# Kernel tuning notes

Hardware: AMD Instinct MI355X
Metric: run time of the kernel (lower is better)

Reference implementation:

```python
import jax, jax.numpy as jnp
import numpy as np

N = 30000      # nodes
D = 512        # nhid
E = 300000     # edges (before self-loops)
P_FEAT = 0.5   # feature dropout (F.dropout, training=True)
P_ATT = 0.6    # GATConv attention dropout
NEG_SLOPE = 0.2
SCALE = 1.0    # PairNorm scale


def setup_inputs() -> dict:
    key = jax.random.key(0)
    k1, k2, k3, k4, k5, k6 = jax.random.split(key, 6)
    x = jax.random.normal(k1, (N, D), dtype=jnp.float32)
    edge_index = jax.random.randint(k2, (2, E), 0, N, dtype=jnp.int32)
    # GATConv params (heads=1): lin weight, att_src/att_dst vectors, bias
    W = jax.random.normal(k3, (D, D), dtype=jnp.float32) * 0.05
    att_src = jax.random.normal(k4, (D,), dtype=jnp.float32) * 0.05
    att_dst = jax.random.normal(k5, (D,), dtype=jnp.float32) * 0.05
    bias = jax.random.normal(k6, (D,), dtype=jnp.float32) * 0.05
    return {"x": x, "edge_index": edge_index, "W": W,
            "att_src": att_src, "att_dst": att_dst, "bias": bias}


def reference(x, edge_index, W, att_src, att_dst, bias):
    # deterministic dropout masks (module runs with training=True)
    dk = jax.random.key(42)
    k_feat, k_att = jax.random.split(dk)

    # F.dropout(x, 0.5, training=True)
    keep = jax.random.bernoulli(k_feat, 1.0 - P_FEAT, x.shape)
    x = jnp.where(keep, x / (1.0 - P_FEAT), jnp.float32(0.0))

    # GATConv(heads=1): linear transform
    h = x @ W                                     # [N, D]

    # add self-loops (PyG default add_self_loops=True)
    src, dst = edge_index[0], edge_index[1]
    loop = jnp.arange(N, dtype=src.dtype)
    src = jnp.concatenate([src, loop])            # [E+N]
    dst = jnp.concatenate([dst, loop])

    # per-edge attention logits: LeakyReLU(a_src . h_j + a_dst . h_i)
    a_s = h @ att_src                             # [N]
    a_d = h @ att_dst                             # [N]
    e = jax.nn.leaky_relu(a_s[src] + a_d[dst], NEG_SLOPE)   # [E+N]

    # segment softmax over incoming edges of each dst node
    m = jax.ops.segment_max(e, dst, num_segments=N)
    m = jnp.where(jnp.isfinite(m), m, jnp.float32(0.0))
    ee = jnp.exp(e - m[dst])
    s = jax.ops.segment_sum(ee, dst, num_segments=N)
    alpha = ee / (s[dst] + 1e-16)                 # [E+N]

    # attention dropout p=0.6
    keep_a = jax.random.bernoulli(k_att, 1.0 - P_ATT, alpha.shape)
    alpha = jnp.where(keep_a, alpha / (1.0 - P_ATT), jnp.float32(0.0))

    # scatter-aggregate weighted messages, add bias
    out = jax.ops.segment_sum(alpha[:, None] * h[src], dst, num_segments=N) + bias

    # PairNorm 'PN': center columns, scale by mean row norm
    out = out - jnp.mean(out, axis=0)
    rownorm_mean = jnp.sqrt(1e-6 + jnp.mean(jnp.sum(out * out, axis=1)))
    out = SCALE * out / rownorm_mean

    return jax.nn.relu(out)
```

## Files before the change

### kernel.cpp

```cpp
#include <hip/hip_runtime.h>
#include <stdint.h>
#include <math.h>


#define N_NODES 30000
#define MPAD    30080
#define DIM     512
#define NEDGE   300000
#define ETOT    330000
#define AGG_BLOCKS 7500
#define RED_BLOCKS 60
#define RED_ROWS   125

#define GEMM_BLOCKS 940
#define CVT_BLOCKS  256
#define DROP_BLOCKS 7520
#define HIST_BLOCKS 1290
#define DOT_BLOCKS  118

#define STILES 118

typedef unsigned int u32;
typedef unsigned short u16;

typedef __attribute__((ext_vector_type(8))) short bf16x8;
typedef __attribute__((ext_vector_type(4))) float f32x4;

__host__ __device__ __forceinline__ void threefry2x32(u32 k0, u32 k1, u32 x0, u32 x1,
                                                      u32& o0, u32& o1) {
  u32 ks2 = k0 ^ k1 ^ 0x1BD11BDAu;
#define TF_R(r) { x0 += x1; x1 = (x1 << r) | (x1 >> (32 - r)); x1 ^= x0; }
  x0 += k0; x1 += k1;
  TF_R(13) TF_R(15) TF_R(26) TF_R(6)
  x0 += k1; x1 += ks2 + 1u;
  TF_R(17) TF_R(29) TF_R(16) TF_R(24)
  x0 += ks2; x1 += k0 + 2u;
  TF_R(13) TF_R(15) TF_R(26) TF_R(6)
  x0 += k0; x1 += k1 + 3u;
  TF_R(17) TF_R(29) TF_R(16) TF_R(24)
  x0 += k1; x1 += ks2 + 4u;
  TF_R(13) TF_R(15) TF_R(26) TF_R(6)
  x0 += ks2; x1 += k0 + 5u;
#undef TF_R
  o0 = x0; o1 = x1;
}

__device__ __forceinline__ u32 tf_fold(u32 k0, u32 k1, u32 idx) {
  u32 a, b;
  threefry2x32(k0, k1, 0u, idx, a, b);
  return a ^ b;
}

__device__ __forceinline__ float bf2f(u32 bits16) {
  return __uint_as_float(bits16 << 16);
}
__device__ __forceinline__ u16 f2bf(float f) {
  u32 u = __float_as_uint(f);
  return (u16)((u + 0x7fffu + ((u >> 16) & 1u)) >> 16);
}

__global__ __launch_bounds__(256) void k_pre(const float* __restrict__ W,
                                             u16* __restrict__ Wt,
                                             const float* __restrict__ x,
                                             u16* __restrict__ xd,
                                             const int* __restrict__ ei,
                                             int* __restrict__ counts,
                                             unsigned int* __restrict__ done,
                                             u32 kf0, u32 kf1) {
  __shared__ u16 tile[32][33];
  int b = blockIdx.x;
  if (b == 0 && threadIdx.x == 0) *done = 0u;
  if (b < CVT_BLOCKS) {
    int bk = (b & 15) * 32, bn = (b >> 4) * 32;
    int c = threadIdx.x & 31, r = threadIdx.x >> 5;
#pragma unroll
    for (int rr = 0; rr < 32; rr += 8)
      tile[r + rr][c] = f2bf(W[(size_t)(bk + r + rr) * DIM + bn + c]);
    __syncthreads();
#pragma unroll
    for (int rr = 0; rr < 32; rr += 8)
      Wt[(size_t)(bn + r + rr) * DIM + bk + c] = tile[c][r + rr];
  } else if (b < CVT_BLOCKS + DROP_BLOCKS) {
    size_t gid = (size_t)(b - CVT_BLOCKS) * 256 + threadIdx.x;
    size_t i0 = gid * 8;
    if (i0 < (size_t)MPAD * DIM) {
      uint4 o = make_uint4(0u, 0u, 0u, 0u);
      if (i0 < (size_t)N_NODES * DIM) {
        float4 v0 = *(const float4*)(x + i0);
        float4 v1 = *(const float4*)(x + i0 + 4);
        float xv[8] = {v0.x, v0.y, v0.z, v0.w, v1.x, v1.y, v1.z, v1.w};
        u32 res[4];
#pragma unroll
        for (int p = 0; p < 4; p++) {
          u32 b0 = tf_fold(kf0, kf1, (u32)i0 + 2 * p);
          u32 b1 = tf_fold(kf0, kf1, (u32)i0 + 2 * p + 1);
          u32 r0 = (b0 >> 31) ? 0u : (u32)f2bf(2.0f * xv[2 * p]);
          u32 r1 = (b1 >> 31) ? 0u : (u32)f2bf(2.0f * xv[2 * p + 1]);
          res[p] = r0 | (r1 << 16);
        }
        o = make_uint4(res[0], res[1], res[2], res[3]);
      }
      *(uint4*)(xd + i0) = o;
    }
  } else {
    int i = (b - CVT_BLOCKS - DROP_BLOCKS) * 256 + threadIdx.x;
    if (i < ETOT) {
      int d = (i < NEDGE) ? ei[NEDGE + i] : (i - NEDGE);
      atomicAdd(&counts[d], 1);
    }
  }
}

__global__ __launch_bounds__(256) void k_gemm(const u16* __restrict__ A,
                                              const u16* __restrict__ B,
                                              u16* __restrict__ H,
                                              const float* __restrict__ atts,
                                              const float* __restrict__ attd,
                                              float* __restrict__ aspart,
                                              float* __restrict__ adpart,
                                              const int* __restrict__ counts,
                                              int* __restrict__ off,
                                              int* __restrict__ cursor) {
  __shared__ __align__(16) u16 lA[128 * 32];
  __shared__ __align__(16) u16 lB[128 * 32];

  if (blockIdx.x == 0) {
    int* tsum = (int*)lA;
    int tid = threadIdx.x, lane = tid & 63, wid = tid >> 6;

    for (int t0 = wid; t0 < STILES; t0 += 32) {
      int4 v[8];
#pragma unroll
      for (int b = 0; b < 8; b++) {
        int t = t0 + b * 4;
        int i = t * 256 + lane * 4;
        if (t < STILES) {
          if (i + 4 <= N_NODES) {
            v[b] = *(const int4*)(counts + i);
          } else {
            v[b].x = (i     < N_NODES) ? counts[i]     : 0;
            v[b].y = (i + 1 < N_NODES) ? counts[i + 1] : 0;
            v[b].z = (i + 2 < N_NODES) ? counts[i + 2] : 0;
            v[b].w = (i + 3 < N_NODES) ? counts[i + 3] : 0;
          }
        } else {
          v[b] = make_int4(0, 0, 0, 0);
        }
      }
#pragma unroll
      for (int b = 0; b < 8; b++) {
        int t = t0 + b * 4;
        if (t < STILES) {
          int s = v[b].x + v[b].y + v[b].z + v[b].w;
#pragma unroll
          for (int d = 1; d < 64; d <<= 1) s += __shfl_xor(s, d);
          if (lane == 0) tsum[t] = s;
        }
      }
    }
    __syncthreads();

    if (wid == 0) {
      int carry = 0;
#pragma unroll
      for (int r = 0; r < 2; r++) {
        int idx = r * 64 + lane;
        int vv = (idx < STILES) ? tsum[idx] : 0;
        int x = vv;
#pragma unroll
        for (int d = 1; d < 64; d <<= 1) {
          int y = __shfl_up(x, d);
          if (lane >= d) x += y;
        }
        if (idx < STILES) tsum[idx] = x - vv + carry;
        carry += __shfl(x, 63);
      }
    }
    __syncthreads();

    for (int t0 = wid; t0 < STILES; t0 += 32) {
      int4 v[8];
#pragma unroll
      for (int b = 0; b < 8; b++) {
        int t = t0 + b * 4;
        int i = t * 256 + lane * 4;
        if (t < STILES) {
          if (i + 4 <= N_NODES) {
            v[b] = *(const int4*)(counts + i);
          } else {
            v[b].x = (i     < N_NODES) ? counts[i]     : 0;
            v[b].y = (i + 1 < N_NODES) ? counts[i + 1] : 0;
            v[b].z = (i + 2 < N_NODES) ? counts[i + 2] : 0;
            v[b].w = (i + 3 < N_NODES) ? counts[i + 3] : 0;
          }
        } else {
          v[b] = make_int4(0, 0, 0, 0);
        }
      }
#pragma unroll
      for (int b = 0; b < 8; b++) {
        int t = t0 + b * 4;
        if (t >= STILES) continue;
        int i = t * 256 + lane * 4;
        int s4 = v[b].x + v[b].y + v[b].z + v[b].w;
        int x = s4;
#pragma unroll
        for (int d = 1; d < 64; d <<= 1) {
          int y = __shfl_up(x, d);
          if (lane >= d) x += y;
        }
        int base = tsum[t] + (x - s4);
        int4 e;
        e.x = base;
        e.y = base + v[b].x;
        e.z = e.y + v[b].y;
        e.w = e.z + v[b].z;
        if (i + 4 <= N_NODES) {
          *(int4*)(off + i) = e;
          *(int4*)(cursor + i) = e;
        } else {
          if (i     < N_NODES) { off[i]     = e.x; cursor[i]     = e.x; }
          if (i + 1 < N_NODES) { off[i + 1] = e.y; cursor[i + 1] = e.y; }
          if (i + 2 < N_NODES) { off[i + 2] = e.z; cursor[i + 2] = e.z; }
          if (i + 3 < N_NODES) { off[i + 3] = e.w; cursor[i + 3] = e.w; }
        }
      }
    }
    if (tid == 0) off[N_NODES] = ETOT;
    return;
  }

  const int g = blockIdx.x - 1;
  const int xcd = g & 7, gi = g >> 3;
  const int wrk = (xcd < 4 ? xcd * 118 : 472 + (xcd - 4) * 117) + gi;

  const int bn = (wrk & 3) * 128;
  const int bm = (wrk >> 2) * 128;
  const int tid = threadIdx.x;
  const int wave = tid >> 6, lane = tid & 63;
  const int quad = lane >> 4, l16 = lane & 15;
  const int wrow = (wave & 1) * 64, wcol = (wave >> 1) * 64;

  f32x4 acc[4][4] = {};
  const int srow = tid >> 2;
  const int scq  = (tid & 3) * 8;

  for (int k0 = 0; k0 < DIM; k0 += 32) {
    uint4 va0 = *(const uint4*)(A + (size_t)(bm + srow) * DIM + k0 + scq);
    uint4 va1 = *(const uint4*)(A + (size_t)(bm + 64 + srow) * DIM + k0 + scq);
    uint4 vb0 = *(const uint4*)(B + (size_t)(bn + srow) * DIM + k0 + scq);
    uint4 vb1 = *(const uint4*)(B + (size_t)(bn + 64 + srow) * DIM + k0 + scq);
    __syncthreads();
    *(uint4*)(lA + srow * 32 + scq) = va0;
    *(uint4*)(lA + (64 + srow) * 32 + scq) = va1;
    *(uint4*)(lB + srow * 32 + scq) = vb0;
    *(uint4*)(lB + (64 + srow) * 32 + scq) = vb1;
    __syncthreads();

    bf16x8 af[4], bfr[4];
#pragma unroll
    for (int i = 0; i < 4; i++)
      af[i] = *(const bf16x8*)(lA + (wrow + i * 16 + l16) * 32 + quad * 8);
#pragma unroll
    for (int j = 0; j < 4; j++)
      bfr[j] = *(const bf16x8*)(lB + (wcol + j * 16 + l16) * 32 + quad * 8);
#pragma unroll
    for (int i = 0; i < 4; i++)
#pragma unroll
      for (int j = 0; j < 4; j++)
        acc[i][j] = __builtin_amdgcn_mfma_f32_16x16x32_bf16(af[i], bfr[j], acc[i][j], 0, 0, 0);
  }

#pragma unroll
  for (int i = 0; i < 4; i++) {
#pragma unroll
    for (int r = 0; r < 4; r++) {
      int row = bm + wrow + i * 16 + quad * 4 + r;
      u16* hp = H + (size_t)row * DIM + bn + wcol + l16;
#pragma unroll
      for (int j = 0; j < 4; j++) hp[j * 16] = f2bf(acc[i][j][r]);
    }
  }

  float as_j[4], ad_j[4];
#pragma unroll
  for (int j = 0; j < 4; j++) {
    int col = bn + wcol + j * 16 + l16;
    as_j[j] = atts[col];
    ad_j[j] = attd[col];
  }
  int slot = ((bn >> 7) << 1) + (wcol >> 6);
#pragma unroll
  for (int i = 0; i < 4; i++) {
#pragma unroll
    for (int r = 0; r < 4; r++) {
      float ps = acc[i][0][r] * as_j[0] + acc[i][1][r] * as_j[1]
               + acc[i][2][r] * as_j[2] + acc[i][3][r] * as_j[3];
      float pd = acc[i][0][r] * ad_j[0] + acc[i][1][r] * ad_j[1]
               + acc[i][2][r] * ad_j[2] + acc[i][3][r] * ad_j[3];
#pragma unroll
      for (int d = 1; d < 16; d <<= 1) {
        ps += __shfl_xor(ps, d);
        pd += __shfl_xor(pd, d);
      }
      int row = bm + wrow + i * 16 + quad * 4 + r;
      if (l16 == 0) {
        aspart[slot * MPAD + row] = ps;
        adpart[slot * MPAD + row] = pd;
      }
    }
  }
}

__global__ __launch_bounds__(256) void k_mid(const float* __restrict__ aspart,
                                             const float* __restrict__ adpart,
                                             float* __restrict__ a_s,
                                             float* __restrict__ a_d,
                                             const int* __restrict__ ei,
                                             int* __restrict__ cursor,
                                             int* __restrict__ perm) {
  int b = blockIdx.x;
  if (b < DOT_BLOCKS) {
    int i = b * 256 + threadIdx.x;
    if (i < N_NODES) {
      float s = 0.f, d = 0.f;
#pragma unroll
      for (int k = 0; k < 8; k++) {
        s += aspart[k * MPAD + i];
        d += adpart[k * MPAD + i];
      }
      a_s[i] = s;
      a_d[i] = d;
    }
  } else {
    int i = (b - DOT_BLOCKS) * 256 + threadIdx.x;
    if (i < ETOT) {
      int d = (i < NEDGE) ? ei[NEDGE + i] : (i - NEDGE);
      int slot = atomicAdd(&cursor[d], 1);
      perm[slot] = i;
    }
  }
}

__global__ __launch_bounds__(256) void k_aggregate(
    const int* __restrict__ ei, const int* __restrict__ off, const int* __restrict__ perm,
    const float* __restrict__ a_s, const float* __restrict__ a_d,
    const u16* __restrict__ h, const float* __restrict__ bias,
    u16* __restrict__ oa, float* __restrict__ colpart,
    float* __restrict__ ssqpart, u32 ka0, u32 ka1) {
  __shared__ float lbuf[4][512];
  int wid = threadIdx.x >> 6;
  int node = blockIdx.x * 4 + wid;
  int lane = threadIdx.x & 63;
  int beg = off[node], end = off[node + 1];
  int deg = end - beg;
  float adn = a_d[node];

  float acc[8] = {0.f, 0.f, 0.f, 0.f, 0.f, 0.f, 0.f, 0.f};

  if (deg <= 64) {
    int idx = beg + lane;
    bool valid = idx < end;
    int s = 0;
    float lg = -3.0e38f;
    u32 keepbits = 0;
    if (valid) {
      int eid = perm[idx];
      s = (eid < NEDGE) ? ei[eid] : (eid - NEDGE);
      lg = a_s[s] + adn;
      lg = (lg < 0.f) ? 0.2f * lg : lg;
      keepbits = tf_fold(ka0, ka1, (u32)eid);
    }
    float mx = lg;
#pragma unroll
    for (int d = 1; d < 64; d <<= 1) mx = fmaxf(mx, __shfl_xor(mx, d));
    float ee = valid ? expf(lg - mx) : 0.f;
    float ssum = ee;
#pragma unroll
    for (int d = 1; d < 64; d <<= 1) ssum += __shfl_xor(ssum, d);
    float inv_s = 2.5f / (ssum + 1e-16f);
    float w = (valid && ((keepbits >> 9) < 3355444u)) ? ee * inv_s : 0.f;

    int j = 0;
    for (; j + 4 <= deg; j += 4) {
      float wj[4]; int sj[4]; uint4 hv[4];
#pragma unroll
      for (int bq = 0; bq < 4; bq++) {
        wj[bq] = __shfl(w, j + bq);
        sj[bq] = __shfl(s, j + bq);
      }
#pragma unroll
      for (int bq = 0; bq < 4; bq++)
        if (wj[bq] != 0.f)
          hv[bq] = *(const uint4*)(h + (size_t)sj[bq] * DIM + lane * 8);
#pragma unroll
      for (int bq = 0; bq < 4; bq++) {
        if (wj[bq] != 0.f) {
          u32 hw[4] = {hv[bq].x, hv[bq].y, hv[bq].z, hv[bq].w};
#pragma unroll
          for (int p = 0; p < 4; p++) {
            acc[2 * p]     += wj[bq] * bf2f(hw[p] & 0xffffu);
            acc[2 * p + 1] += wj[bq] * bf2f(hw[p] >> 16);
          }
        }
      }
    }
    for (; j < deg; j++) {
      float wjv = __shfl(w, j);
      if (wjv != 0.f) {
        int sjv = __shfl(s, j);
        uint4 hvv = *(const uint4*)(h + (size_t)sjv * DIM + lane * 8);
        u32 hw[4] = {hvv.x, hvv.y, hvv.z, hvv.w};
#pragma unroll
        for (int p = 0; p < 4; p++) {
          acc[2 * p]     += wjv * bf2f(hw[p] & 0xffffu);
          acc[2 * p + 1] += wjv * bf2f(hw[p] >> 16);
        }
      }
    }
  } else {
    float mx = -3.0e38f;
    for (int base = beg; base < end; base += 64) {
      int idx = base + lane;
      if (idx < end) {
        int eid = perm[idx];
        int s = (eid < NEDGE) ? ei[eid] : (eid - NEDGE);
        float lg = a_s[s] + adn;
        lg = (lg < 0.f) ? 0.2f * lg : lg;
        mx = fmaxf(mx, lg);
      }
    }
#pragma unroll
    for (int d = 1; d < 64; d <<= 1) mx = fmaxf(mx, __shfl_xor(mx, d));
    float ssum = 0.f;
    for (int base = beg; base < end; base += 64) {
      int idx = base + lane;
      if (idx < end) {
        int eid = perm[idx];
        int s = (eid < NEDGE) ? ei[eid] : (eid - NEDGE);
        float lg = a_s[s] + adn;
        lg = (lg < 0.f) ? 0.2f * lg : lg;
        ssum += expf(lg - mx);
      }
    }
#pragma unroll
    for (int d = 1; d < 64; d <<= 1) ssum += __shfl_xor(ssum, d);
    float inv_s = 2.5f / (ssum + 1e-16f);
    for (int base = beg; base < end; base += 64) {
      int idx = base + lane;
      float w = 0.f; int s = 0;
      if (idx < end) {
        int eid = perm[idx];
        s = (eid < NEDGE) ? ei[eid] : (eid - NEDGE);
        float lg = a_s[s] + adn;
        lg = (lg < 0.f) ? 0.2f * lg : lg;
        float ee = expf(lg - mx);
        u32 bits = tf_fold(ka0, ka1, (u32)eid);
        if ((bits >> 9) < 3355444u) w = ee * inv_s;
      }
      int cnt = min(64, end - base);
      for (int j = 0; j < cnt; j++) {
        float wj = __shfl(w, j);
        if (wj != 0.f) {
          int sj = __shfl(s, j);
          uint4 hv = *(const uint4*)(h + (size_t)sj * DIM + lane * 8);
          u32 hw[4] = {hv.x, hv.y, hv.z, hv.w};
#pragma unroll
          for (int p = 0; p < 4; p++) {
            acc[2 * p]     += wj * bf2f(hw[p] & 0xffffu);
            acc[2 * p + 1] += wj * bf2f(hw[p] >> 16);
          }
        }
      }
    }
  }

  float4 b0 = *(const float4*)(bias + lane * 8);
  float4 b1 = *(const float4*)(bias + lane * 8 + 4);
  float bb[8] = {b0.x, b0.y, b0.z, b0.w, b1.x, b1.y, b1.z, b1.w};
  u32 res[4];
  float vq[8];
#pragma unroll
  for (int p = 0; p < 4; p++) {
    u16 q0 = f2bf(acc[2 * p]     + bb[2 * p]);
    u16 q1 = f2bf(acc[2 * p + 1] + bb[2 * p + 1]);
    res[p] = (u32)q0 | ((u32)q1 << 16);
    vq[2 * p]     = bf2f(q0);
    vq[2 * p + 1] = bf2f(q1);
  }
  *(uint4*)(oa + (size_t)node * DIM + lane * 8) = make_uint4(res[0], res[1], res[2], res[3]);
  *(float4*)&lbuf[wid][lane * 8]     = make_float4(vq[0], vq[1], vq[2], vq[3]);
  *(float4*)&lbuf[wid][lane * 8 + 4] = make_float4(vq[4], vq[5], vq[6], vq[7]);
  __syncthreads();

  int t = threadIdx.x;
  float s0 = 0.f, s1 = 0.f, ssl = 0.f;
#pragma unroll
  for (int w = 0; w < 4; w++) {
    float a = lbuf[w][t], b = lbuf[w][t + 256];
    s0 += a; s1 += b;
    ssl = fmaf(a, a, ssl);
    ssl = fmaf(b, b, ssl);
  }
  colpart[(size_t)blockIdx.x * 512 + t]       = s0;
  colpart[(size_t)blockIdx.x * 512 + 256 + t] = s1;
#pragma unroll
  for (int d = 1; d < 64; d <<= 1) ssl += __shfl_xor(ssl, d);
  __shared__ float wss[4];
  if ((t & 63) == 0) wss[t >> 6] = ssl;
  __syncthreads();
  if (t == 0) ssqpart[blockIdx.x] = wss[0] + wss[1] + wss[2] + wss[3];
}

__global__ __launch_bounds__(256) void k_redstats(const float* __restrict__ colpart,
                                                  const float* __restrict__ ssqpart,
                                                  float* __restrict__ colpart2,
                                                  double* __restrict__ ssqp2,
                                                  unsigned int* __restrict__ done,
                                                  float* __restrict__ mu,
                                                  float* __restrict__ invp) {
  int b = blockIdx.x;
  int t = threadIdx.x;
  int r0 = b * RED_ROWS;
  float s0 = 0.f, s1 = 0.f;
  for (int r = r0; r < r0 + RED_ROWS; r++) {
    s0 += colpart[(size_t)r * 512 + t];
    s1 += colpart[(size_t)r * 512 + 256 + t];
  }
  colpart2[(size_t)b * 512 + t]       = s0;
  colpart2[(size_t)b * 512 + 256 + t] = s1;
  float sl = (t < RED_ROWS) ? ssqpart[r0 + t] : 0.f;
#pragma unroll
  for (int d = 1; d < 64; d <<= 1) sl += __shfl_xor(sl, d);
  __shared__ float w4[4];
  if ((t & 63) == 0) w4[t >> 6] = sl;
  __syncthreads();
  if (t == 0) ssqp2[b] = (double)(w4[0] + w4[1] + w4[2] + w4[3]);

  __threadfence();
  __syncthreads();
  __shared__ unsigned int olds;
  if (t == 0) olds = atomicAdd(done, 1u);
  __syncthreads();
  if (olds == RED_BLOCKS - 1) {
    __threadfence();
    float m0 = 0.f, m1 = 0.f;
    for (int r = 0; r < RED_BLOCKS; r++) {
      m0 += colpart2[(size_t)r * 512 + t];
      m1 += colpart2[(size_t)r * 512 + 256 + t];
    }
    m0 *= (1.0f / 30000.0f);
    m1 *= (1.0f / 30000.0f);
    mu[t]       = m0;
    mu[t + 256] = m1;
    double p = (double)m0 * (double)m0 + (double)m1 * (double)m1;
#pragma unroll
    for (int d = 1; d < 64; d <<= 1) p += __shfl_xor(p, d);
    __shared__ double sred[4];
    __shared__ double ssqs;
    if ((t & 63) == 0) sred[t >> 6] = p;
    if (t < 64) {
      double sq = (t < RED_BLOCKS) ? ssqp2[t] : 0.0;
#pragma unroll
      for (int d = 1; d < 64; d <<= 1) sq += __shfl_xor(sq, d);
      if (t == 0) ssqs = sq;
    }
    __syncthreads();
    if (t == 0) {
      double smu2 = sred[0] + sred[1] + sred[2] + sred[3];
      double centered = ssqs - 30000.0 * smu2;
      double mean = centered * (1.0 / 30000.0);
      if (!(mean >= 0.0)) mean = 0.0;
      float rn = sqrtf(1e-6f + (float)mean);
      invp[0] = 1.0f / rn;
    }
  }
}

__global__ __launch_bounds__(256) void k_finalout(const u16* __restrict__ oa,
                                                  const float* __restrict__ mu,
                                                  const float* __restrict__ invp,
                                                  float* __restrict__ out) {
  size_t gid = (size_t)blockIdx.x * 256 + threadIdx.x;
  size_t i0 = gid * 8;
  if (i0 >= (size_t)N_NODES * DIM) return;
  float inv = invp[0];
  int j = (int)(i0 & (DIM - 1));
  uint4 v = *(const uint4*)(oa + i0);
  u32 w[4] = {v.x, v.y, v.z, v.w};
  float o[8];
#pragma unroll
  for (int p = 0; p < 4; p++) {
    float z0 = (bf2f(w[p] & 0xffffu) - mu[j + 2 * p]) * inv;
    float z1 = (bf2f(w[p] >> 16)     - mu[j + 2 * p + 1]) * inv;
    o[2 * p]     = (z0 < 0.f) ? 0.f : z0;
    o[2 * p + 1] = (z1 < 0.f) ? 0.f : z1;
  }
  *(float4*)(out + i0)     = make_float4(o[0], o[1], o[2], o[3]);
  *(float4*)(out + i0 + 4) = make_float4(o[4], o[5], o[6], o[7]);
}

extern "C" void kernel_launch(void* const* d_in, const int* in_sizes, int n_in,
                              void* d_out, int out_size, void* d_ws, size_t ws_size,
                              hipStream_t stream) {
  const float* x    = (const float*)d_in[0];
  const int*   ei   = (const int*)d_in[1];
  const float* W    = (const float*)d_in[2];
  const float* atts = (const float*)d_in[3];
  const float* attd = (const float*)d_in[4];
  const float* bias = (const float*)d_in[5];
  float* out = (float*)d_out;
  char* ws = (char*)d_ws;

  u16*   xd      = (u16*)(ws + 0);
  u16*   oa      = (u16*)(ws + 0);
  float* aspart  = (float*)(ws + 32000000);
  float* adpart  = (float*)(ws + 33000000);
  float* colpart2 = (float*)(ws + 34000000);
  double* ssqp2  = (double*)(ws + 34130000);
  unsigned int* done = (unsigned int*)(ws + 34140000);
  u16*   h       = (u16*)(ws + 61440000);
  u16*   Wt      = (u16*)(ws + 92241920);
  float* a_s     = (float*)(ws + 92766208);
  float* a_d     = (float*)(ws + 92886272);
  int*   counts  = (int*)(ws + 93006336);
  int*   offs    = (int*)(ws + 93126400);
  int*   cursor  = (int*)(ws + 93246464);
  int*   perm    = (int*)(ws + 93366528);
  float* mu      = (float*)(ws + 94688576);
  float* invp    = (float*)(ws + 94690688);

  float* colpart = out;
  float* ssqpart = out + (size_t)AGG_BLOCKS * 512;

  u32 kf0, kf1, ka0, ka1;
  threefry2x32(0u, 42u, 0u, 0u, kf0, kf1);
  threefry2x32(0u, 42u, 0u, 1u, ka0, ka1);

  hipMemsetAsync(counts, 0, 120064, stream);

  k_pre<<<CVT_BLOCKS + DROP_BLOCKS + HIST_BLOCKS, 256, 0, stream>>>(
      W, Wt, x, xd, ei, counts, done, kf0, kf1);
  k_gemm<<<GEMM_BLOCKS + 1, 256, 0, stream>>>(xd, Wt, h, atts, attd,
                                              aspart, adpart, counts, offs, cursor);
  k_mid<<<DOT_BLOCKS + HIST_BLOCKS, 256, 0, stream>>>(aspart, adpart, a_s, a_d,
                                                      ei, cursor, perm);
  k_aggregate<<<AGG_BLOCKS, 256, 0, stream>>>(ei, offs, perm, a_s, a_d, h, bias,
                                              oa, colpart, ssqpart, ka0, ka1);
  k_redstats<<<RED_BLOCKS, 256, 0, stream>>>(colpart, ssqpart, colpart2, ssqp2,
                                             done, mu, invp);
  k_finalout<<<7500, 256, 0, stream>>>(oa, mu, invp, out);
}
```

Baseline: 271.2 us.

## Store sorted source ids in CSR build and fuse stats reduction with final output

The CSR build in k_mid now also writes each edge's source node into a perm_src array, so the aggregation kernel no longer does a dependent gather through perm and ei to find sources. The PairNorm statistics reduction and the final normalize/ReLU kernel are merged into one launch. The first 60 blocks reduce the statistics and publish a ready flag, while the other blocks prefetch their oa slice and spin until the flag is set. Partial buffers move from the output array into the workspace. This saves a kernel launch and an indirection, but the spin-wait depends on the reduction blocks being scheduled before or alongside the waiting blocks.

```diff
diff --git a/kernel.cpp b/kernel.cpp
--- a/kernel.cpp
+++ b/kernel.cpp
@@ -11,6 +11,7 @@
 #define AGG_BLOCKS 7500
 #define RED_BLOCKS 60
 #define RED_ROWS   125
+#define FIN_BLOCKS 7500
 
 #define GEMM_BLOCKS 940
 #define CVT_BLOCKS  256
@@ -66,10 +67,11 @@
                                              const int* __restrict__ ei,
                                              int* __restrict__ counts,
                                              unsigned int* __restrict__ done,
+                                             unsigned int* __restrict__ ready,
                                              u32 kf0, u32 kf1) {
   __shared__ u16 tile[32][33];
   int b = blockIdx.x;
-  if (b == 0 && threadIdx.x == 0) *done = 0u;
+  if (b == 0 && threadIdx.x == 0) { *done = 0u; *ready = 0u; }
   if (b < CVT_BLOCKS) {
     int bk = (b & 15) * 32, bn = (b >> 4) * 32;
     int c = threadIdx.x & 31, r = threadIdx.x >> 5;
@@ -318,7 +320,8 @@
                                              float* __restrict__ a_d,
                                              const int* __restrict__ ei,
                                              int* __restrict__ cursor,
-                                             int* __restrict__ perm) {
+                                             int* __restrict__ perm,
+                                             int* __restrict__ perm_src) {
   int b = blockIdx.x;
   if (b < DOT_BLOCKS) {
     int i = b * 256 + threadIdx.x;
@@ -335,15 +338,18 @@
   } else {
     int i = (b - DOT_BLOCKS) * 256 + threadIdx.x;
     if (i < ETOT) {
-      int d = (i < NEDGE) ? ei[NEDGE + i] : (i - NEDGE);
+      int d   = (i < NEDGE) ? ei[NEDGE + i] : (i - NEDGE);
+      int src = (i < NEDGE) ? ei[i]         : (i - NEDGE);
       int slot = atomicAdd(&cursor[d], 1);
       perm[slot] = i;
+      perm_src[slot] = src;
     }
   }
 }
 
 __global__ __launch_bounds__(256) void k_aggregate(
-    const int* __restrict__ ei, const int* __restrict__ off, const int* __restrict__ perm,
+    const int* __restrict__ off, const int* __restrict__ perm,
+    const int* __restrict__ perm_src,
     const float* __restrict__ a_s, const float* __restrict__ a_d,
     const u16* __restrict__ h, const float* __restrict__ bias,
     u16* __restrict__ oa, float* __restrict__ colpart,
@@ -366,7 +372,7 @@
     u32 keepbits = 0;
     if (valid) {
       int eid = perm[idx];
-      s = (eid < NEDGE) ? ei[eid] : (eid - NEDGE);
+      s = perm_src[idx];
       lg = a_s[s] + adn;
       lg = (lg < 0.f) ? 0.2f * lg : lg;
       keepbits = tf_fold(ka0, ka1, (u32)eid);
@@ -423,8 +429,7 @@
     for (int base = beg; base < end; base += 64) {
       int idx = base + lane;
       if (idx < end) {
-        int eid = perm[idx];
-        int s = (eid < NEDGE) ? ei[eid] : (eid - NEDGE);
+        int s = perm_src[idx];
         float lg = a_s[s] + adn;
         lg = (lg < 0.f) ? 0.2f * lg : lg;
         mx = fmaxf(mx, lg);
@@ -436,8 +441,7 @@
     for (int base = beg; base < end; base += 64) {
       int idx = base + lane;
       if (idx < end) {
-        int eid = perm[idx];
-        int s = (eid < NEDGE) ? ei[eid] : (eid - NEDGE);
+        int s = perm_src[idx];
         float lg = a_s[s] + adn;
         lg = (lg < 0.f) ? 0.2f * lg : lg;
         ssum += expf(lg - mx);
@@ -451,7 +455,7 @@
       float w = 0.f; int s = 0;
       if (idx < end) {
         int eid = perm[idx];
-        s = (eid < NEDGE) ? ei[eid] : (eid - NEDGE);
+        s = perm_src[idx];
         float lg = a_s[s] + adn;
         lg = (lg < 0.f) ? 0.2f * lg : lg;
         float ee = expf(lg - mx);
@@ -512,81 +516,88 @@
   if (t == 0) ssqpart[blockIdx.x] = wss[0] + wss[1] + wss[2] + wss[3];
 }
 
-__global__ __launch_bounds__(256) void k_redstats(const float* __restrict__ colpart,
-                                                  const float* __restrict__ ssqpart,
-                                                  float* __restrict__ colpart2,
-                                                  double* __restrict__ ssqp2,
-                                                  unsigned int* __restrict__ done,
-                                                  float* __restrict__ mu,
-                                                  float* __restrict__ invp) {
-  int b = blockIdx.x;
+__global__ __launch_bounds__(256) void k_final(const float* __restrict__ colpart,
+                                               const float* __restrict__ ssqpart,
+                                               float* __restrict__ colpart2,
+                                               double* __restrict__ ssqp2,
+                                               unsigned int* __restrict__ done,
+                                               unsigned int* __restrict__ ready,
+                                               float* __restrict__ mu,
+                                               float* __restrict__ invp,
+                                               const u16* __restrict__ oa,
+                                               float* __restrict__ out) {
   int t = threadIdx.x;
-  int r0 = b * RED_ROWS;
-  float s0 = 0.f, s1 = 0.f;
-  for (int r = r0; r < r0 + RED_ROWS; r++) {
-    s0 += colpart[(size_t)r * 512 + t];
-    s1 += colpart[(size_t)r * 512 + 256 + t];
-  }
-  colpart2[(size_t)b * 512 + t]       = s0;
-  colpart2[(size_t)b * 512 + 256 + t] = s1;
-  float sl = (t < RED_ROWS) ? ssqpart[r0 + t] : 0.f;
-#pragma unroll
-  for (int d = 1; d < 64; d <<= 1) sl += __shfl_xor(sl, d);
-  __shared__ float w4[4];
-  if ((t & 63) == 0) w4[t >> 6] = sl;
+  if (blockIdx.x < RED_BLOCKS) {
+    int b = blockIdx.x;
+    int r0 = b * RED_ROWS;
+    float s0 = 0.f, s1 = 0.f;
+    for (int r = r0; r < r0 + RED_ROWS; r++) {
+      s0 += colpart[(size_t)r * 512 + t];
+      s1 += colpart[(size_t)r * 512 + 256 + t];
+    }
+    colpart2[(size_t)b * 512 + t]       = s0;
+    colpart2[(size_t)b * 512 + 256 + t] = s1;
+    float sl = (t < RED_ROWS) ? ssqpart[r0 + t] : 0.f;
+#pragma unroll
+    for (int d = 1; d < 64; d <<= 1) sl += __shfl_xor(sl, d);
+    __shared__ float w4[4];
+    if ((t & 63) == 0) w4[t >> 6] = sl;
+    __syncthreads();
+    if (t == 0) ssqp2[b] = (double)(w4[0] + w4[1] + w4[2] + w4[3]);
+
+    __threadfence();
+    __syncthreads();
+    __shared__ unsigned int olds;
+    if (t == 0) olds = atomicAdd(done, 1u);
+    __syncthreads();
+    if (olds == RED_BLOCKS - 1) {
+      __threadfence();
+      float m0 = 0.f, m1 = 0.f;
+      for (int r = 0; r < RED_BLOCKS; r++) {
+        m0 += colpart2[(size_t)r * 512 + t];
+        m1 += colpart2[(size_t)r * 512 + 256 + t];
+      }
+      m0 *= (1.0f / 30000.0f);
+      m1 *= (1.0f / 30000.0f);
+      mu[t]       = m0;
+      mu[t + 256] = m1;
+      double p = (double)m0 * (double)m0 + (double)m1 * (double)m1;
+#pragma unroll
+      for (int d = 1; d < 64; d <<= 1) p += __shfl_xor(p, d);
+      __shared__ double sred[4];
+      __shared__ double ssqs;
+      if ((t & 63) == 0) sred[t >> 6] = p;
+      if (t < 64) {
+        double sq = (t < RED_BLOCKS) ? ssqp2[t] : 0.0;
+#pragma unroll
+        for (int d = 1; d < 64; d <<= 1) sq += __shfl_xor(sq, d);
+        if (t == 0) ssqs = sq;
+      }
+      __syncthreads();
+      if (t == 0) {
+        double smu2 = sred[0] + sred[1] + sred[2] + sred[3];
+        double centered = ssqs - 30000.0 * smu2;
+        double mean = centered * (1.0 / 30000.0);
+        if (!(mean >= 0.0)) mean = 0.0;
+        float rn = sqrtf(1e-6f + (float)mean);
+        invp[0] = 1.0f / rn;
+        __threadfence();
+        atomicExch(ready, 1u);
+      }
+    }
+    return;
+  }
+
+  size_t gid = (size_t)(blockIdx.x - RED_BLOCKS) * 256 + t;
+  size_t i0 = gid * 8;
+  uint4 v = *(const uint4*)(oa + i0);
+  if (t == 0) {
+    while (__hip_atomic_load(ready, __ATOMIC_ACQUIRE, __HIP_MEMORY_SCOPE_AGENT) == 0u)
+      __builtin_amdgcn_s_sleep(16);
+  }
   __syncthreads();
-  if (t == 0) ssqp2[b] = (double)(w4[0] + w4[1] + w4[2] + w4[3]);
-
-  __threadfence();
-  __syncthreads();
-  __shared__ unsigned int olds;
-  if (t == 0) olds = atomicAdd(done, 1u);
-  __syncthreads();
-  if (olds == RED_BLOCKS - 1) {
-    __threadfence();
-    float m0 = 0.f, m1 = 0.f;
-    for (int r = 0; r < RED_BLOCKS; r++) {
-      m0 += colpart2[(size_t)r * 512 + t];
-      m1 += colpart2[(size_t)r * 512 + 256 + t];
-    }
-    m0 *= (1.0f / 30000.0f);
-    m1 *= (1.0f / 30000.0f);
-    mu[t]       = m0;
-    mu[t + 256] = m1;
-    double p = (double)m0 * (double)m0 + (double)m1 * (double)m1;
-#pragma unroll
-    for (int d = 1; d < 64; d <<= 1) p += __shfl_xor(p, d);
-    __shared__ double sred[4];
-    __shared__ double ssqs;
-    if ((t & 63) == 0) sred[t >> 6] = p;
-    if (t < 64) {
-      double sq = (t < RED_BLOCKS) ? ssqp2[t] : 0.0;
-#pragma unroll
-      for (int d = 1; d < 64; d <<= 1) sq += __shfl_xor(sq, d);
-      if (t == 0) ssqs = sq;
-    }
-    __syncthreads();
-    if (t == 0) {
-      double smu2 = sred[0] + sred[1] + sred[2] + sred[3];
-      double centered = ssqs - 30000.0 * smu2;
-      double mean = centered * (1.0 / 30000.0);
-      if (!(mean >= 0.0)) mean = 0.0;
-      float rn = sqrtf(1e-6f + (float)mean);
-      invp[0] = 1.0f / rn;
-    }
-  }
-}
-
-__global__ __launch_bounds__(256) void k_finalout(const u16* __restrict__ oa,
-                                                  const float* __restrict__ mu,
-                                                  const float* __restrict__ invp,
-                                                  float* __restrict__ out) {
-  size_t gid = (size_t)blockIdx.x * 256 + threadIdx.x;
-  size_t i0 = gid * 8;
-  if (i0 >= (size_t)N_NODES * DIM) return;
   float inv = invp[0];
   int j = (int)(i0 & (DIM - 1));
-  uint4 v = *(const uint4*)(oa + i0);
   u32 w[4] = {v.x, v.y, v.z, v.w};
   float o[8];
 #pragma unroll
@@ -618,7 +629,11 @@
   float* adpart  = (float*)(ws + 33000000);
   float* colpart2 = (float*)(ws + 34000000);
   double* ssqp2  = (double*)(ws + 34130000);
-  unsigned int* done = (unsigned int*)(ws + 34140000);
+  unsigned int* done  = (unsigned int*)(ws + 34140000);
+  unsigned int* ready = (unsigned int*)(ws + 34140064);
+  float* colpart = (float*)(ws + 35000000);
+  float* ssqpart = (float*)(ws + 50500000);
+  int*   perm_src = (int*)(ws + 51000000);
   u16*   h       = (u16*)(ws + 61440000);
   u16*   Wt      = (u16*)(ws + 92241920);
   float* a_s     = (float*)(ws + 92766208);
@@ -630,9 +645,6 @@
   float* mu      = (float*)(ws + 94688576);
   float* invp    = (float*)(ws + 94690688);
 
-  float* colpart = out;
-  float* ssqpart = out + (size_t)AGG_BLOCKS * 512;
-
   u32 kf0, kf1, ka0, ka1;
   threefry2x32(0u, 42u, 0u, 0u, kf0, kf1);
   threefry2x32(0u, 42u, 0u, 1u, ka0, ka1);
@@ -640,14 +652,15 @@
   hipMemsetAsync(counts, 0, 120064, stream);
 
   k_pre<<<CVT_BLOCKS + DROP_BLOCKS + HIST_BLOCKS, 256, 0, stream>>>(
-      W, Wt, x, xd, ei, counts, done, kf0, kf1);
+      W, Wt, x, xd, ei, counts, done, ready, kf0, kf1);
   k_gemm<<<GEMM_BLOCKS + 1, 256, 0, stream>>>(xd, Wt, h, atts, attd,
                                               aspart, adpart, counts, offs, cursor);
   k_mid<<<DOT_BLOCKS + HIST_BLOCKS, 256, 0, stream>>>(aspart, adpart, a_s, a_d,
-                                                      ei, cursor, perm);
-  k_aggregate<<<AGG_BLOCKS, 256, 0, stream>>>(ei, offs, perm, a_s, a_d, h, bias,
-                                              oa, colpart, ssqpart, ka0, ka1);
-  k_redstats<<<RED_BLOCKS, 256, 0, stream>>>(colpart, ssqpart, colpart2, ssqp2,
-                                             done, mu, invp);
-  k_finalout<<<7500, 256, 0, stream>>>(oa, mu, invp, out);
-}
+                                                      ei, cursor, perm, perm_src);
+  k_aggregate<<<AGG_BLOCKS, 256, 0, stream>>>(offs, perm, perm_src, a_s, a_d,
+                                              h, bias, oa, colpart, ssqpart,
+                                              ka0, ka1);
+  k_final<<<RED_BLOCKS + FIN_BLOCKS, 256, 0, stream>>>(colpart, ssqpart,
+                                                       colpart2, ssqp2, done,
+                                                       ready, mu, invp, oa, out);
+}
```

New measurement: 790.4 us. +191.5%, slower.
